# Kernel tuning notes

Measured on AMD Instinct MI355X. Metric: run time of the kernel, lower is better.

## Reference

```python
import jax, jax.numpy as jnp
import numpy as np

N_NODES = 100000
N_EDGES = 1600000
IN_F = 128
OUT_F = 64


def setup_inputs() -> dict:
    key = jax.random.key(0)
    ks = jax.random.split(key, 9)
    x = jax.random.normal(ks[0], (N_NODES, IN_F), dtype=jnp.float32)
    Wv = jax.random.normal(ks[1], (IN_F, OUT_F), dtype=jnp.float32) / np.sqrt(IN_F)
    bv = jax.random.normal(ks[2], (OUT_F,), dtype=jnp.float32) * 0.02
    wq = jax.random.normal(ks[3], (OUT_F,), dtype=jnp.float32) / np.sqrt(OUT_F)
    bq = jax.random.normal(ks[4], (1,), dtype=jnp.float32) * 0.02
    wk = jax.random.normal(ks[5], (OUT_F,), dtype=jnp.float32) / np.sqrt(OUT_F)
    bk = jax.random.normal(ks[6], (1,), dtype=jnp.float32) * 0.02
    src = jax.random.randint(ks[7], (N_EDGES,), 0, N_NODES, dtype=jnp.int64)
    dst = jax.random.randint(ks[8], (N_EDGES,), 0, N_NODES, dtype=jnp.int64)
    return {"x": x, "Wv": Wv, "bv": bv, "wq": wq, "bq": bq,
            "wk": wk, "bk": bk, "src": src, "dst": dst}


def reference(x, Wv, bv, wq, bq, wk, bk, src, dst):
    n = x.shape[0]
    # node transform (linear_v) and scalar scores (linear_q, linear_k)
    xv = x @ Wv + bv                      # [N, OUT_F]
    el = xv @ wq + bq[0]                  # [N] source score
    er = xv @ wk + bk[0]                  # [N] destination score
    # per-edge score: u_add_v + leaky_relu(0.2)
    e = jax.nn.leaky_relu(el[src] + er[dst], negative_slope=0.2)  # [E]
    # edge softmax over incoming edges of each dst (numerically stable)
    emax = jax.ops.segment_max(e, dst, num_segments=n)            # [N]
    ex = jnp.exp(e - emax[dst])                                   # [E]
    denom = jax.ops.segment_sum(ex, dst, num_segments=n)          # [N]
    attn = ex / denom[dst]                                        # [E]
    # u_mul_e + aggregate_sum: weighted scatter of source features into dst
    out = jax.ops.segment_sum(xv[src] * attn[:, None], dst, num_segments=n)
    return out
```

## Files before the change

### kernel.cpp

```cpp
#include <hip/hip_runtime.h>
#include <hip/hip_bf16.h>

#define NN 100000
#define NE 1600000
#define IN_F 128
#define OUT_F 64
#define NBINS 782
#define BIN_SHIFT 7
#define GEMM_WGS 1563
#define P1_WGS 391
#define NREP2 8
#define SUBCAP 384

typedef __attribute__((ext_vector_type(8))) short bf16x8;
typedef __attribute__((ext_vector_type(4))) float f32x4;

__device__ __forceinline__ short f2bf(float f) {
  unsigned u = __float_as_uint(f);
  unsigned r = (u + 0x7fffu + ((u >> 16) & 1u)) >> 16;
  return (short)r;
}
__device__ __forceinline__ float bf2f(ushort u) {
  return __uint_as_float(((unsigned)u) << 16);
}

__global__ __launch_bounds__(256) void prep_w(
    const float* __restrict__ Wv, short* __restrict__ wvt,
    int* __restrict__ bincur) {
  if (blockIdx.x == 0)
    for (int i = threadIdx.x; i < NREP2 * NBINS; i += 256) bincur[i] = 0;
  const int i = blockIdx.x * 256 + threadIdx.x;
  if (i >= IN_F * OUT_F) return;
  const int j = i >> 7, k = i & 127;
  wvt[i] = f2bf(Wv[k * OUT_F + j]);
}

__global__ __launch_bounds__(256) void fused_tp(
    const float* __restrict__ x, const short* __restrict__ wvt,
    const float* __restrict__ bv, const float* __restrict__ wq,
    const float* __restrict__ bq, const float* __restrict__ wk,
    const float* __restrict__ bk,
    ushort* __restrict__ xvb, float* __restrict__ el, float* __restrict__ er,
    const int* __restrict__ src, const int* __restrict__ dst,
    int* __restrict__ bincur, unsigned* __restrict__ slab) {
  if (blockIdx.x >= GEMM_WGS) {
    __shared__ int hist[NBINS];
    __shared__ int base_[NBINS];
    const int pb = blockIdx.x - GEMM_WGS;
    const int t = threadIdx.x;
    const int rep = pb & (NREP2 - 1);
    for (int i = t; i < NBINS; i += 256) hist[i] = 0;
    __syncthreads();
    const int e0 = pb * 4096;
    int sv[16], dv[16];
#pragma unroll
    for (int r = 0; r < 16; ++r) {
      const int i = e0 + r * 256 + t;
      if (i < NE) {
        sv[r] = src[i];
        dv[r] = dst[i];
        atomicAdd(&hist[dv[r] >> BIN_SHIFT], 1);
      } else {
        sv[r] = -1;
        dv[r] = 0;
      }
    }
    __syncthreads();
    for (int b = t; b < NBINS; b += 256) {
      base_[b] = (hist[b] > 0) ? atomicAdd(&bincur[rep * NBINS + b], hist[b]) : 0;
      hist[b] = 0;
    }
    __syncthreads();
#pragma unroll
    for (int r = 0; r < 16; ++r) {
      if (sv[r] >= 0) {
        const int s = sv[r], d = dv[r];
        const int b = d >> BIN_SHIFT;
        const unsigned dl = (unsigned)(d & 127);
        const int pos = base_[b] + atomicAdd(&hist[b], 1);
        slab[(size_t)(b * NREP2 + rep) * SUBCAP + pos] = (dl << 17) | (unsigned)s;
      }
    }
    return;
  }

  const int wave = threadIdx.x >> 6, lane = threadIdx.x & 63;
  const int node0 = blockIdx.x * 64 + wave * 16;
  const int j15 = lane & 15, g = lane >> 4;
  const int kb = g * 8;

  int row = node0 + j15;
  if (row >= NN) row = NN - 1;
  const float* xr = x + (size_t)row * IN_F;
  bf16x8 a[4];
#pragma unroll
  for (int kt = 0; kt < 4; ++kt) {
    const float4 f0 = *(const float4*)(xr + kt * 32 + kb);
    const float4 f1 = *(const float4*)(xr + kt * 32 + kb + 4);
    bf16x8 t;
    t[0] = f2bf(f0.x); t[1] = f2bf(f0.y); t[2] = f2bf(f0.z); t[3] = f2bf(f0.w);
    t[4] = f2bf(f1.x); t[5] = f2bf(f1.y); t[6] = f2bf(f1.z); t[7] = f2bf(f1.w);
    a[kt] = t;
  }

  bf16x8 b[16];
#pragma unroll
  for (int nt = 0; nt < 4; ++nt)
#pragma unroll
    for (int kt = 0; kt < 4; ++kt)
      b[nt * 4 + kt] = *(const bf16x8*)(wvt + (size_t)(nt * 16 + j15) * IN_F + kt * 32 + kb);

  f32x4 acc[4];
#pragma unroll
  for (int nt = 0; nt < 4; ++nt) acc[nt] = (f32x4){0.f, 0.f, 0.f, 0.f};
#pragma unroll
  for (int nt = 0; nt < 4; ++nt)
#pragma unroll
    for (int kt = 0; kt < 4; ++kt)
      acc[nt] = __builtin_amdgcn_mfma_f32_16x16x32_bf16(a[kt], b[nt * 4 + kt], acc[nt], 0, 0, 0);

  float bvl[4], wql[4], wkl[4];
#pragma unroll
  for (int nt = 0; nt < 4; ++nt) {
    bvl[nt] = bv[nt * 16 + j15];
    wql[nt] = wq[nt * 16 + j15];
    wkl[nt] = wk[nt * 16 + j15];
  }
  const float bq0 = bq[0], bk0 = bk[0];

#pragma unroll
  for (int r = 0; r < 4; ++r) {
    const int node = node0 + g * 4 + r;
    float pq = 0.f, pk = 0.f;
#pragma unroll
    for (int nt = 0; nt < 4; ++nt) {
      const float v = acc[nt][r] + bvl[nt];
      if (node < NN) xvb[(size_t)node * OUT_F + nt * 16 + j15] = (ushort)f2bf(v);
      pq += v * wql[nt];
      pk += v * wkl[nt];
    }
#pragma unroll
    for (int o = 1; o < 16; o <<= 1) {
      pq += __shfl_xor(pq, o);
      pk += __shfl_xor(pk, o);
    }
    if (j15 == 0 && node < NN) {
      el[node] = pq + bq0;
      er[node] = pk + bk0;
    }
  }
}

__global__ __launch_bounds__(256) void bin_scatter(
    const unsigned* __restrict__ slab, const int* __restrict__ bincur,
    const float* __restrict__ el, const float* __restrict__ er,
    int* __restrict__ off, uint2* __restrict__ csr) {
  __shared__ int sp[256];
  __shared__ int cnt[128];
  __shared__ float er_l[128];
  __shared__ int s_csr0;
  const int b = blockIdx.x, t = threadIdx.x;
  const int n0 = b << BIN_SHIFT;

  int v = 0;
#pragma unroll
  for (int j = 0; j < 4; ++j) {
    const int bb = 4 * t + j;
    if (bb < NBINS) {
#pragma unroll
      for (int r = 0; r < NREP2; ++r) v += bincur[r * NBINS + bb];
    }
  }
  sp[t] = v;
  __syncthreads();
  for (int o = 1; o < 256; o <<= 1) {
    const int u = (t >= o) ? sp[t - o] : 0;
    __syncthreads();
    sp[t] += u;
    __syncthreads();
  }
  if (t == 0) {
    const int q = b >> 2, rr = b & 3;
    int c = (q > 0) ? sp[q - 1] : 0;
    for (int j = 0; j < rr; ++j)
      for (int r = 0; r < NREP2; ++r) c += bincur[r * NBINS + (4 * q + j)];
    s_csr0 = c;
  }
  if (t < 128) {
    cnt[t] = 0;
    const int n = n0 + t;
    er_l[t] = (n < NN) ? er[n] : 0.f;
  }
  __syncthreads();
  const int csr0 = s_csr0;

#pragma unroll
  for (int rep = 0; rep < NREP2; ++rep) {
    const int c = bincur[rep * NBINS + b];
    const unsigned* sl = slab + (size_t)(b * NREP2 + rep) * SUBCAP;
    for (int i = t; i < c; i += 256)
      atomicAdd(&cnt[sl[i] >> 17], 1);
  }
  __syncthreads();

  const int cme = (t < 128) ? cnt[t] : 0;
  sp[t] = cme;
  __syncthreads();
  for (int o = 1; o < 128; o <<= 1) {
    const int u = (t >= o && t < 128) ? sp[t - o] : 0;
    __syncthreads();
    if (t < 128) sp[t] += u;
    __syncthreads();
  }
  if (t < 128) {
    const int cur = csr0 + sp[t] - cme;
    cnt[t] = cur;
    if (n0 + t < NN) off[n0 + t] = cur;
  }
  if (b == NBINS - 1 && t == 0) off[NN] = NE;
  __syncthreads();

#pragma unroll
  for (int rep = 0; rep < NREP2; ++rep) {
    const int c = bincur[rep * NBINS + b];
    const unsigned* sl = slab + (size_t)(b * NREP2 + rep) * SUBCAP;
    for (int i = t; i < c; i += 256) {
      const unsigned w = sl[i];
      const int dl = (int)(w >> 17);
      const int s = (int)(w & 0x1FFFFu);
      float e = el[s] + er_l[dl];
      e = e > 0.f ? e : 0.2f * e;
      const int pos = atomicAdd(&cnt[dl], 1);
      csr[pos] = (uint2){(unsigned)s, __float_as_uint(e)};
    }
  }
}

__global__ __launch_bounds__(256) void node_aggregate(
    const ushort* __restrict__ xvb, const int* __restrict__ off,
    const uint2* __restrict__ csr, float* __restrict__ out) {
  const int wave = threadIdx.x >> 6, lane = threadIdx.x & 63;
  const int node = blockIdx.x * 4 + wave;
  if (node >= NN) return;
  const int base = off[node];
  const int deg = off[node + 1] - base;

  if (deg <= 64) {
    const bool valid = lane < deg;
    uint2 w = valid ? csr[base + lane] : (uint2){0u, 0u};
    int s = (int)w.x;
    float p = valid ? __expf(__uint_as_float(w.y)) : 0.f;
    float t = p;
#pragma unroll
    for (int o = 32; o; o >>= 1) t += __shfl_xor(t, o);
    p *= (deg > 0) ? (1.0f / t) : 0.f;

    const int fgrp = lane & 7, egrp = lane >> 3;
    float4 aLo = {0.f, 0.f, 0.f, 0.f};
    float4 aHi = {0.f, 0.f, 0.f, 0.f};
    const int nr = (deg + 7) >> 3;
#pragma unroll 4
    for (int r = 0; r < nr; ++r) {
      const int k = (r << 3) + egrp;
      const int sk = __shfl(s, k);
      const float pk = __shfl(p, k);
      if (k < deg) {
        const uint4 v = *(const uint4*)(xvb + (size_t)sk * OUT_F + (fgrp << 3));
        aLo.x += pk * __uint_as_float(v.x << 16);
        aLo.y += pk * __uint_as_float(v.x & 0xffff0000u);
        aLo.z += pk * __uint_as_float(v.y << 16);
        aLo.w += pk * __uint_as_float(v.y & 0xffff0000u);
        aHi.x += pk * __uint_as_float(v.z << 16);
        aHi.y += pk * __uint_as_float(v.z & 0xffff0000u);
        aHi.z += pk * __uint_as_float(v.w << 16);
        aHi.w += pk * __uint_as_float(v.w & 0xffff0000u);
      }
    }
#pragma unroll
    for (int o = 8; o <= 32; o <<= 1) {
      aLo.x += __shfl_xor(aLo.x, o);
      aLo.y += __shfl_xor(aLo.y, o);
      aLo.z += __shfl_xor(aLo.z, o);
      aLo.w += __shfl_xor(aLo.w, o);
      aHi.x += __shfl_xor(aHi.x, o);
      aHi.y += __shfl_xor(aHi.y, o);
      aHi.z += __shfl_xor(aHi.z, o);
      aHi.w += __shfl_xor(aHi.w, o);
    }
    if (egrp == 0) {
      float* op = out + (size_t)node * OUT_F + (fgrp << 3);
      *(float4*)op = aLo;
      *(float4*)(op + 4) = aHi;
    }
  } else {
    float m = -3.0e38f;
    for (int k = lane; k < deg; k += 64) m = fmaxf(m, __uint_as_float(csr[base + k].y));
#pragma unroll
    for (int o = 32; o; o >>= 1) m = fmaxf(m, __shfl_xor(m, o));
    float ssum = 0.f;
    for (int k = lane; k < deg; k += 64) ssum += __expf(__uint_as_float(csr[base + k].y) - m);
#pragma unroll
    for (int o = 32; o; o >>= 1) ssum += __shfl_xor(ssum, o);
    const float inv = 1.0f / ssum;
    float acc = 0.f;
    for (int k = 0; k < deg; ++k) {
      const uint2 w = csr[base + k];
      const float pk = __expf(__uint_as_float(w.y) - m) * inv;
      acc += pk * bf2f(xvb[(size_t)w.x * OUT_F + lane]);
    }
    out[(size_t)node * OUT_F + lane] = acc;
  }
}

extern "C" void kernel_launch(void* const* d_in, const int* in_sizes, int n_in,
                              void* d_out, int out_size, void* d_ws, size_t ws_size,
                              hipStream_t stream) {
  const float* x  = (const float*)d_in[0];
  const float* Wv = (const float*)d_in[1];
  const float* bv = (const float*)d_in[2];
  const float* wq = (const float*)d_in[3];
  const float* bq = (const float*)d_in[4];
  const float* wk = (const float*)d_in[5];
  const float* bk = (const float*)d_in[6];
  const int* src  = (const int*)d_in[7];
  const int* dst  = (const int*)d_in[8];
  float* out = (float*)d_out;

  ushort* xvb = (ushort*)d_ws;
  float* el = (float*)(xvb + (size_t)NN * OUT_F);
  float* er = el + NN;
  int* off = (int*)(er + NN);
  uint2* csr = (uint2*)(off + NN + 2);
  unsigned* slab = (unsigned*)(csr + NE);
  short* wvt = (short*)(slab + (size_t)NBINS * NREP2 * SUBCAP);
  int* bincur = (int*)(wvt + IN_F * OUT_F);

  prep_w<<<(IN_F * OUT_F + 255) / 256, 256, 0, stream>>>(Wv, wvt, bincur);
  fused_tp<<<GEMM_WGS + P1_WGS, 256, 0, stream>>>(x, wvt, bv, wq, bq, wk, bk,
                                                  xvb, el, er, src, dst, bincur, slab);
  bin_scatter<<<NBINS, 256, 0, stream>>>(slab, bincur, el, er, off, csr);
  node_aggregate<<<(NN + 3) / 4, 256, 0, stream>>>(xvb, off, csr, out);
}
```

Before: 116.5 us.

## Fuse bin scatter and node aggregation into one kernel using LDS-resident CSR

```diff
diff --git a/kernel.cpp b/kernel.cpp
--- a/kernel.cpp
+++ b/kernel.cpp
@@ -11,6 +11,7 @@
 #define P1_WGS 391
 #define NREP2 8
 #define SUBCAP 384
+#define BINCAP (NREP2 * SUBCAP)
 
 typedef __attribute__((ext_vector_type(8))) short bf16x8;
 typedef __attribute__((ext_vector_type(4))) float f32x4;
@@ -151,59 +152,38 @@
   }
 }
 
-__global__ __launch_bounds__(256) void bin_scatter(
+__global__ __launch_bounds__(256) void bin_aggregate(
     const unsigned* __restrict__ slab, const int* __restrict__ bincur,
     const float* __restrict__ el, const float* __restrict__ er,
-    int* __restrict__ off, uint2* __restrict__ csr) {
+    const ushort* __restrict__ xvb, float* __restrict__ out) {
+  __shared__ uint2 recs[BINCAP];
+  __shared__ int sbase[129];
+  __shared__ int cur[128];
+  __shared__ float er_l[128];
   __shared__ int sp[256];
-  __shared__ int cnt[128];
-  __shared__ float er_l[128];
-  __shared__ int s_csr0;
   const int b = blockIdx.x, t = threadIdx.x;
   const int n0 = b << BIN_SHIFT;
 
-  int v = 0;
-#pragma unroll
-  for (int j = 0; j < 4; ++j) {
-    const int bb = 4 * t + j;
-    if (bb < NBINS) {
-#pragma unroll
-      for (int r = 0; r < NREP2; ++r) v += bincur[r * NBINS + bb];
-    }
-  }
-  sp[t] = v;
-  __syncthreads();
-  for (int o = 1; o < 256; o <<= 1) {
-    const int u = (t >= o) ? sp[t - o] : 0;
-    __syncthreads();
-    sp[t] += u;
-    __syncthreads();
-  }
-  if (t == 0) {
-    const int q = b >> 2, rr = b & 3;
-    int c = (q > 0) ? sp[q - 1] : 0;
-    for (int j = 0; j < rr; ++j)
-      for (int r = 0; r < NREP2; ++r) c += bincur[r * NBINS + (4 * q + j)];
-    s_csr0 = c;
-  }
   if (t < 128) {
-    cnt[t] = 0;
+    cur[t] = 0;
     const int n = n0 + t;
     er_l[t] = (n < NN) ? er[n] : 0.f;
   }
   __syncthreads();
-  const int csr0 = s_csr0;
+
+  int repcnt[NREP2];
+#pragma unroll
+  for (int r = 0; r < NREP2; ++r) repcnt[r] = bincur[r * NBINS + b];
 
 #pragma unroll
   for (int rep = 0; rep < NREP2; ++rep) {
-    const int c = bincur[rep * NBINS + b];
     const unsigned* sl = slab + (size_t)(b * NREP2 + rep) * SUBCAP;
-    for (int i = t; i < c; i += 256)
-      atomicAdd(&cnt[sl[i] >> 17], 1);
-  }
-  __syncthreads();
-
-  const int cme = (t < 128) ? cnt[t] : 0;
+    for (int i = t; i < repcnt[rep]; i += 256)
+      atomicAdd(&cur[sl[i] >> 17], 1);
+  }
+  __syncthreads();
+
+  const int cme = (t < 128) ? cur[t] : 0;
   sp[t] = cme;
   __syncthreads();
   for (int o = 1; o < 128; o <<= 1) {
@@ -213,102 +193,99 @@
     __syncthreads();
   }
   if (t < 128) {
-    const int cur = csr0 + sp[t] - cme;
-    cnt[t] = cur;
-    if (n0 + t < NN) off[n0 + t] = cur;
-  }
-  if (b == NBINS - 1 && t == 0) off[NN] = NE;
+    sbase[t] = sp[t] - cme;
+    cur[t] = sp[t] - cme;
+  }
+  if (t == 127) sbase[128] = sp[127];
   __syncthreads();
 
 #pragma unroll
   for (int rep = 0; rep < NREP2; ++rep) {
-    const int c = bincur[rep * NBINS + b];
     const unsigned* sl = slab + (size_t)(b * NREP2 + rep) * SUBCAP;
-    for (int i = t; i < c; i += 256) {
+    for (int i = t; i < repcnt[rep]; i += 256) {
       const unsigned w = sl[i];
       const int dl = (int)(w >> 17);
       const int s = (int)(w & 0x1FFFFu);
       float e = el[s] + er_l[dl];
       e = e > 0.f ? e : 0.2f * e;
-      const int pos = atomicAdd(&cnt[dl], 1);
-      csr[pos] = (uint2){(unsigned)s, __float_as_uint(e)};
-    }
-  }
-}
-
-__global__ __launch_bounds__(256) void node_aggregate(
-    const ushort* __restrict__ xvb, const int* __restrict__ off,
-    const uint2* __restrict__ csr, float* __restrict__ out) {
-  const int wave = threadIdx.x >> 6, lane = threadIdx.x & 63;
-  const int node = blockIdx.x * 4 + wave;
-  if (node >= NN) return;
-  const int base = off[node];
-  const int deg = off[node + 1] - base;
-
-  if (deg <= 64) {
-    const bool valid = lane < deg;
-    uint2 w = valid ? csr[base + lane] : (uint2){0u, 0u};
-    int s = (int)w.x;
-    float p = valid ? __expf(__uint_as_float(w.y)) : 0.f;
-    float t = p;
-#pragma unroll
-    for (int o = 32; o; o >>= 1) t += __shfl_xor(t, o);
-    p *= (deg > 0) ? (1.0f / t) : 0.f;
-
-    const int fgrp = lane & 7, egrp = lane >> 3;
-    float4 aLo = {0.f, 0.f, 0.f, 0.f};
-    float4 aHi = {0.f, 0.f, 0.f, 0.f};
-    const int nr = (deg + 7) >> 3;
+      const int pos = atomicAdd(&cur[dl], 1);
+      recs[pos] = (uint2){(unsigned)s, __float_as_uint(e)};
+    }
+  }
+  __syncthreads();
+
+  const int wave = t >> 6, lane = t & 63;
+  for (int n = wave; n < 128; n += 4) {
+    const int node = n0 + n;
+    if (node >= NN) break;
+    const int base = sbase[n];
+    const int deg = sbase[n + 1] - base;
+
+    if (deg <= 64) {
+      const bool valid = lane < deg;
+      uint2 w = valid ? recs[base + lane] : (uint2){0u, 0u};
+      int s = (int)w.x;
+      float p = valid ? __expf(__uint_as_float(w.y)) : 0.f;
+      float tt = p;
+#pragma unroll
+      for (int o = 32; o; o >>= 1) tt += __shfl_xor(tt, o);
+      p *= (deg > 0) ? (1.0f / tt) : 0.f;
+
+      const int fgrp = lane & 7, egrp = lane >> 3;
+      float4 aLo = {0.f, 0.f, 0.f, 0.f};
+      float4 aHi = {0.f, 0.f, 0.f, 0.f};
+      const int nr = (deg + 7) >> 3;
 #pragma unroll 4
-    for (int r = 0; r < nr; ++r) {
-      const int k = (r << 3) + egrp;
-      const int sk = __shfl(s, k);
-      const float pk = __shfl(p, k);
-      if (k < deg) {
-        const uint4 v = *(const uint4*)(xvb + (size_t)sk * OUT_F + (fgrp << 3));
-        aLo.x += pk * __uint_as_float(v.x << 16);
-        aLo.y += pk * __uint_as_float(v.x & 0xffff0000u);
-        aLo.z += pk * __uint_as_float(v.y << 16);
-        aLo.w += pk * __uint_as_float(v.y & 0xffff0000u);
-        aHi.x += pk * __uint_as_float(v.z << 16);
-        aHi.y += pk * __uint_as_float(v.z & 0xffff0000u);
-        aHi.z += pk * __uint_as_float(v.w << 16);
-        aHi.w += pk * __uint_as_float(v.w & 0xffff0000u);
-      }
-    }
-#pragma unroll
-    for (int o = 8; o <= 32; o <<= 1) {
-      aLo.x += __shfl_xor(aLo.x, o);
-      aLo.y += __shfl_xor(aLo.y, o);
-      aLo.z += __shfl_xor(aLo.z, o);
-      aLo.w += __shfl_xor(aLo.w, o);
-      aHi.x += __shfl_xor(aHi.x, o);
-      aHi.y += __shfl_xor(aHi.y, o);
-      aHi.z += __shfl_xor(aHi.z, o);
-      aHi.w += __shfl_xor(aHi.w, o);
-    }
-    if (egrp == 0) {
-      float* op = out + (size_t)node * OUT_F + (fgrp << 3);
-      *(float4*)op = aLo;
-      *(float4*)(op + 4) = aHi;
-    }
-  } else {
-    float m = -3.0e38f;
-    for (int k = lane; k < deg; k += 64) m = fmaxf(m, __uint_as_float(csr[base + k].y));
-#pragma unroll
-    for (int o = 32; o; o >>= 1) m = fmaxf(m, __shfl_xor(m, o));
-    float ssum = 0.f;
-    for (int k = lane; k < deg; k += 64) ssum += __expf(__uint_as_float(csr[base + k].y) - m);
-#pragma unroll
-    for (int o = 32; o; o >>= 1) ssum += __shfl_xor(ssum, o);
-    const float inv = 1.0f / ssum;
-    float acc = 0.f;
-    for (int k = 0; k < deg; ++k) {
-      const uint2 w = csr[base + k];
-      const float pk = __expf(__uint_as_float(w.y) - m) * inv;
-      acc += pk * bf2f(xvb[(size_t)w.x * OUT_F + lane]);
-    }
-    out[(size_t)node * OUT_F + lane] = acc;
+      for (int r = 0; r < nr; ++r) {
+        const int k = (r << 3) + egrp;
+        const int sk = __shfl(s, k);
+        const float pk = __shfl(p, k);
+        if (k < deg) {
+          const uint4 v = *(const uint4*)(xvb + (size_t)sk * OUT_F + (fgrp << 3));
+          aLo.x += pk * __uint_as_float(v.x << 16);
+          aLo.y += pk * __uint_as_float(v.x & 0xffff0000u);
+          aLo.z += pk * __uint_as_float(v.y << 16);
+          aLo.w += pk * __uint_as_float(v.y & 0xffff0000u);
+          aHi.x += pk * __uint_as_float(v.z << 16);
+          aHi.y += pk * __uint_as_float(v.z & 0xffff0000u);
+          aHi.z += pk * __uint_as_float(v.w << 16);
+          aHi.w += pk * __uint_as_float(v.w & 0xffff0000u);
+        }
+      }
+#pragma unroll
+      for (int o = 8; o <= 32; o <<= 1) {
+        aLo.x += __shfl_xor(aLo.x, o);
+        aLo.y += __shfl_xor(aLo.y, o);
+        aLo.z += __shfl_xor(aLo.z, o);
+        aLo.w += __shfl_xor(aLo.w, o);
+        aHi.x += __shfl_xor(aHi.x, o);
+        aHi.y += __shfl_xor(aHi.y, o);
+        aHi.z += __shfl_xor(aHi.z, o);
+        aHi.w += __shfl_xor(aHi.w, o);
+      }
+      if (egrp == 0) {
+        float* op = out + (size_t)node * OUT_F + (fgrp << 3);
+        *(float4*)op = aLo;
+        *(float4*)(op + 4) = aHi;
+      }
+    } else {
+      float m = -3.0e38f;
+      for (int k = lane; k < deg; k += 64) m = fmaxf(m, __uint_as_float(recs[base + k].y));
+#pragma unroll
+      for (int o = 32; o; o >>= 1) m = fmaxf(m, __shfl_xor(m, o));
+      float ssum = 0.f;
+      for (int k = lane; k < deg; k += 64) ssum += __expf(__uint_as_float(recs[base + k].y) - m);
+#pragma unroll
+      for (int o = 32; o; o >>= 1) ssum += __shfl_xor(ssum, o);
+      const float inv = 1.0f / ssum;
+      float acc = 0.f;
+      for (int k = 0; k < deg; ++k) {
+        const uint2 w = recs[base + k];
+        const float pk = __expf(__uint_as_float(w.y) - m) * inv;
+        acc += pk * bf2f(xvb[(size_t)w.x * OUT_F + lane]);
+      }
+      out[(size_t)node * OUT_F + lane] = acc;
+    }
   }
 }
 
@@ -329,15 +306,12 @@
   ushort* xvb = (ushort*)d_ws;
   float* el = (float*)(xvb + (size_t)NN * OUT_F);
   float* er = el + NN;
-  int* off = (int*)(er + NN);
-  uint2* csr = (uint2*)(off + NN + 2);
-  unsigned* slab = (unsigned*)(csr + NE);
+  unsigned* slab = (unsigned*)(er + NN);
   short* wvt = (short*)(slab + (size_t)NBINS * NREP2 * SUBCAP);
   int* bincur = (int*)(wvt + IN_F * OUT_F);
 
   prep_w<<<(IN_F * OUT_F + 255) / 256, 256, 0, stream>>>(Wv, wvt, bincur);
   fused_tp<<<GEMM_WGS + P1_WGS, 256, 0, stream>>>(x, wvt, bv, wq, bq, wk, bk,
                                                   xvb, el, er, src, dst, bincur, slab);
-  bin_scatter<<<NBINS, 256, 0, stream>>>(slab, bincur, el, er, off, csr);
-  node_aggregate<<<(NN + 3) / 4, 256, 0, stream>>>(xvb, off, csr, out);
-}
+  bin_aggregate<<<NBINS, 256, 0, stream>>>(slab, bincur, el, er, xvb, out);
+}
```

New measurement: 124.9 us. 1.07x slower.

## Stage x tile in LDS and split GEMM output columns across waves

Applied to the files above, without the earlier changes.

```diff
diff --git a/kernel.cpp b/kernel.cpp
--- a/kernel.cpp
+++ b/kernel.cpp
@@ -11,6 +11,7 @@
 #define P1_WGS 391
 #define NREP2 8
 #define SUBCAP 384
+#define XS_STRIDE 132
 
 typedef __attribute__((ext_vector_type(8))) short bf16x8;
 typedef __attribute__((ext_vector_type(4))) float f32x4;
@@ -43,10 +44,11 @@
     ushort* __restrict__ xvb, float* __restrict__ el, float* __restrict__ er,
     const int* __restrict__ src, const int* __restrict__ dst,
     int* __restrict__ bincur, unsigned* __restrict__ slab) {
-  if (blockIdx.x >= GEMM_WGS) {
-    __shared__ int hist[NBINS];
-    __shared__ int base_[NBINS];
-    const int pb = blockIdx.x - GEMM_WGS;
+  __shared__ __align__(16) char smem_[36352];
+  if (blockIdx.x < P1_WGS) {
+    int* hist = (int*)smem_;
+    int* base_ = hist + NBINS;
+    const int pb = blockIdx.x;
     const int t = threadIdx.x;
     const int rep = pb & (NREP2 - 1);
     for (int i = t; i < NBINS; i += 256) hist[i] = 0;
@@ -84,69 +86,75 @@
     return;
   }
 
-  const int wave = threadIdx.x >> 6, lane = threadIdx.x & 63;
-  const int node0 = blockIdx.x * 64 + wave * 16;
+  float* xs = (float*)smem_;
+  float* pql = (float*)(smem_ + 64 * XS_STRIDE * 4);
+  float* pkl = pql + 256;
+  const int gb = blockIdx.x - P1_WGS;
+  const int node0 = gb * 64;
+  const int t = threadIdx.x;
+  const int wave = t >> 6, lane = t & 63;
   const int j15 = lane & 15, g = lane >> 4;
-  const int kb = g * 8;
-
-  int row = node0 + j15;
-  if (row >= NN) row = NN - 1;
-  const float* xr = x + (size_t)row * IN_F;
-  bf16x8 a[4];
-#pragma unroll
-  for (int kt = 0; kt < 4; ++kt) {
-    const float4 f0 = *(const float4*)(xr + kt * 32 + kb);
-    const float4 f1 = *(const float4*)(xr + kt * 32 + kb + 4);
-    bf16x8 t;
-    t[0] = f2bf(f0.x); t[1] = f2bf(f0.y); t[2] = f2bf(f0.z); t[3] = f2bf(f0.w);
-    t[4] = f2bf(f1.x); t[5] = f2bf(f1.y); t[6] = f2bf(f1.z); t[7] = f2bf(f1.w);
-    a[kt] = t;
-  }
-
-  bf16x8 b[16];
-#pragma unroll
-  for (int nt = 0; nt < 4; ++nt)
-#pragma unroll
-    for (int kt = 0; kt < 4; ++kt)
-      b[nt * 4 + kt] = *(const bf16x8*)(wvt + (size_t)(nt * 16 + j15) * IN_F + kt * 32 + kb);
-
-  f32x4 acc[4];
-#pragma unroll
-  for (int nt = 0; nt < 4; ++nt) acc[nt] = (f32x4){0.f, 0.f, 0.f, 0.f};
-#pragma unroll
-  for (int nt = 0; nt < 4; ++nt)
-#pragma unroll
-    for (int kt = 0; kt < 4; ++kt)
-      acc[nt] = __builtin_amdgcn_mfma_f32_16x16x32_bf16(a[kt], b[nt * 4 + kt], acc[nt], 0, 0, 0);
-
-  float bvl[4], wql[4], wkl[4];
-#pragma unroll
-  for (int nt = 0; nt < 4; ++nt) {
-    bvl[nt] = bv[nt * 16 + j15];
-    wql[nt] = wq[nt * 16 + j15];
-    wkl[nt] = wk[nt * 16 + j15];
-  }
+
+#pragma unroll
+  for (int i = 0; i < 8; ++i) {
+    const int idx = i * 256 + t;
+    const int row = idx >> 5, col4 = (idx & 31) << 2;
+    int grow = node0 + row;
+    if (grow >= NN) grow = NN - 1;
+    const float4 v = *(const float4*)(x + (size_t)grow * IN_F + col4);
+    *(float4*)(xs + row * XS_STRIDE + col4) = v;
+  }
+
+  const int nt = wave;
+  bf16x8 b[4];
+#pragma unroll
+  for (int kt = 0; kt < 4; ++kt)
+    b[kt] = *(const bf16x8*)(wvt + (size_t)(nt * 16 + j15) * IN_F + kt * 32 + g * 8);
+
+  const float bvl = bv[nt * 16 + j15];
+  const float wql = wq[nt * 16 + j15];
+  const float wkl = wk[nt * 16 + j15];
   const float bq0 = bq[0], bk0 = bk[0];
 
-#pragma unroll
-  for (int r = 0; r < 4; ++r) {
-    const int node = node0 + g * 4 + r;
-    float pq = 0.f, pk = 0.f;
-#pragma unroll
-    for (int nt = 0; nt < 4; ++nt) {
-      const float v = acc[nt][r] + bvl[nt];
+  __syncthreads();
+
+#pragma unroll
+  for (int ntile = 0; ntile < 4; ++ntile) {
+    f32x4 acc = (f32x4){0.f, 0.f, 0.f, 0.f};
+#pragma unroll
+    for (int kt = 0; kt < 4; ++kt) {
+      const float* ap = xs + (ntile * 16 + j15) * XS_STRIDE + kt * 32 + g * 8;
+      const float4 f0 = *(const float4*)ap;
+      const float4 f1 = *(const float4*)(ap + 4);
+      bf16x8 a;
+      a[0] = f2bf(f0.x); a[1] = f2bf(f0.y); a[2] = f2bf(f0.z); a[3] = f2bf(f0.w);
+      a[4] = f2bf(f1.x); a[5] = f2bf(f1.y); a[6] = f2bf(f1.z); a[7] = f2bf(f1.w);
+      acc = __builtin_amdgcn_mfma_f32_16x16x32_bf16(a, b[kt], acc, 0, 0, 0);
+    }
+#pragma unroll
+    for (int r = 0; r < 4; ++r) {
+      const int nl = ntile * 16 + g * 4 + r;
+      const int node = node0 + nl;
+      const float v = acc[r] + bvl;
       if (node < NN) xvb[(size_t)node * OUT_F + nt * 16 + j15] = (ushort)f2bf(v);
-      pq += v * wql[nt];
-      pk += v * wkl[nt];
-    }
-#pragma unroll
-    for (int o = 1; o < 16; o <<= 1) {
-      pq += __shfl_xor(pq, o);
-      pk += __shfl_xor(pk, o);
-    }
-    if (j15 == 0 && node < NN) {
-      el[node] = pq + bq0;
-      er[node] = pk + bk0;
+      float pq = v * wql, pk = v * wkl;
+#pragma unroll
+      for (int o = 1; o < 16; o <<= 1) {
+        pq += __shfl_xor(pq, o);
+        pk += __shfl_xor(pk, o);
+      }
+      if (j15 == 0) {
+        pql[nl * 4 + nt] = pq;
+        pkl[nl * 4 + nt] = pk;
+      }
+    }
+  }
+  __syncthreads();
+  if (t < 64) {
+    const int node = node0 + t;
+    if (node < NN) {
+      el[node] = pql[t * 4] + pql[t * 4 + 1] + pql[t * 4 + 2] + pql[t * 4 + 3] + bq0;
+      er[node] = pkl[t * 4] + pkl[t * 4 + 1] + pkl[t * 4 + 2] + pkl[t * 4 + 3] + bk0;
     }
   }
 }
@@ -336,7 +344,7 @@
   int* bincur = (int*)(wvt + IN_F * OUT_F);
 
   prep_w<<<(IN_F * OUT_F + 255) / 256, 256, 0, stream>>>(Wv, wvt, bincur);
-  fused_tp<<<GEMM_WGS + P1_WGS, 256, 0, stream>>>(x, wvt, bv, wq, bq, wk, bk,
+  fused_tp<<<P1_WGS + GEMM_WGS, 256, 0, stream>>>(x, wvt, bv, wq, bq, wk, bk,
                                                   xvb, el, er, src, dst, bincur, slab);
   bin_scatter<<<NBINS, 256, 0, stream>>>(slab, bincur, el, er, off, csr);
   node_aggregate<<<(NN + 3) / 4, 256, 0, stream>>>(xvb, off, csr, out);
```

Result: faster. 109.8 us (-5.8%).
